# Kernel tuning notes

Hardware: AMD Instinct MI355X
Metric: run time of the kernel (lower is better)

## Reference

```python
import jax, jax.numpy as jnp
import numpy as np

TOPK_RATIO = 0.2
DICE_WEIGHT = 0.5
SHAPE = (2, 1, 128, 192, 192)


def setup_inputs() -> dict:
    key = jax.random.key(0)
    k1, k2 = jax.random.split(key)
    logits = jax.random.normal(k1, SHAPE, dtype=jnp.float32)
    targets = jax.random.uniform(k2, SHAPE, dtype=jnp.float32)
    return {"logits": logits, "targets": targets}


def _bce_with_logits(x, t):
    # stable: max(x,0) - x*t + log(1+exp(-|x|))
    return jnp.maximum(x, 0.0) - x * t + jnp.log1p(jnp.exp(-jnp.abs(x)))


def reference(logits, targets):
    # --- TopK BCE ---
    flat_loss = _bce_with_logits(logits, targets).reshape(-1)
    n = flat_loss.shape[0]
    k_samples = max(1, int(n * TOPK_RATIO))
    topk_losses, _ = jax.lax.top_k(flat_loss, k_samples)
    bce = jnp.mean(topk_losses)

    # --- Soft Dice ---
    p = jax.nn.sigmoid(logits).reshape(-1)
    t = targets.reshape(-1)
    intersection = jnp.sum(p * t)
    union = jnp.sum(p) + jnp.sum(t)
    dice = (2.0 * intersection + 1e-06) / (union + 1e-06)
    dice_loss = 1.0 - dice

    return bce + DICE_WEIGHT * dice_loss
```

## Files before the change

### kernel.cpp

```cpp
#include <hip/hip_runtime.h>
#include <math.h>
#include <limits.h>

#define NB1 8192
#define NB2 4096
#define VEC 4

__device__ __forceinline__ void elem_f(float x, float t, float& l, float& p) {
    float e = __expf(-fabsf(x));
    l = fmaxf(x, 0.f) - x * t + __logf(1.f + e);
    float r = __builtin_amdgcn_rcpf(1.f + e);
    p = (x >= 0.f) ? r : e * r;
}

__global__ __launch_bounds__(256) void sample_kernel(
    const float4* __restrict__ x4, const float4* __restrict__ t4,
    unsigned* __restrict__ H1, int n4)
{
    __shared__ unsigned lh[NB1];
    for (int i = threadIdx.x; i < NB1; i += 256) lh[i] = 0u;
    __syncthreads();
    int tid = blockIdx.x * 256 + threadIdx.x;
    int stride = gridDim.x * 256;
    int S4 = n4 >> 4;
    for (int i = tid; i < S4; i += stride) {
        int f4 = ((i >> 6) << 10) + (i & 63);
        if (f4 >= n4) continue;
        float4 xv = x4[f4];
        float4 tv = t4[f4];
        float xs[4] = {xv.x, xv.y, xv.z, xv.w};
        float ts[4] = {tv.x, tv.y, tv.z, tv.w};
        #pragma unroll
        for (int c = 0; c < 4; ++c) {
            float l, p;
            elem_f(xs[c], ts[c], l, p);
            atomicAdd(&lh[__float_as_uint(l) >> 19], 1u);
        }
    }
    __syncthreads();
    for (int i = threadIdx.x; i < NB1; i += 256) {
        unsigned c = lh[i];
        if (c) atomicAdd(&H1[i], c);
    }
}

__global__ __launch_bounds__(256) void band_kernel(
    const unsigned* __restrict__ H1, float* __restrict__ band,
    long long ks, long long M)
{
    __shared__ unsigned lh[NB1];
    const uint4* hv = (const uint4*)H1;
    uint4* lv = (uint4*)lh;
    for (int i = threadIdx.x; i < NB1 / 4; i += 256) lv[i] = hv[i];
    __syncthreads();
    if (threadIdx.x >= 64) return;

    int lane = threadIdx.x;
    int base = lane << 7;
    unsigned long long chunk = 0;
    for (int j = 0; j < 128; ++j) chunk += lh[base + j];
    unsigned long long s = chunk;
    #pragma unroll
    for (int off = 1; off < 64; off <<= 1) {
        unsigned long long v = __shfl_down(s, off);
        if (lane + off < 64) s += v;
    }
    unsigned long long above = s - chunk;

    int my_bhi = INT_MAX, my_blo = -1;
    unsigned long long c = above;
    for (int j = 127; j >= 0; --j) {
        unsigned h = lh[base + j];
        if ((long long)(c + h) < ks - M) my_bhi = base + j;
        if ((long long)c > ks + M && my_blo < 0) my_blo = base + j;
        c += h;
    }
    #pragma unroll
    for (int off = 32; off; off >>= 1) {
        int a = __shfl_down(my_bhi, off); my_bhi = min(my_bhi, a);
        int b = __shfl_down(my_blo, off); my_blo = max(my_blo, b);
    }
    if (lane == 0) {
        int bhi = (my_bhi == INT_MAX) ? (NB1 - 1) : my_bhi;
        int blo = my_blo;
        float vhi = __uint_as_float((unsigned)bhi << 19);
        float vlo = (blo < 0) ? 0.f : __uint_as_float((unsigned)(blo + 1) << 19);
        if (!(vlo < vhi)) vlo = 0.f;
        band[0] = vlo;
        band[1] = vhi;
    }
}

__device__ __forceinline__ void process4(
    float4 xv, float4 tv, float vlo, float vhi, float scale,
    float& sp, float& spt, float& st, float& sgt, unsigned& cnt,
    unsigned* __restrict__ hist2)
{
    float xs[4] = {xv.x, xv.y, xv.z, xv.w};
    float ts[4] = {tv.x, tv.y, tv.z, tv.w};
    #pragma unroll
    for (int c = 0; c < 4; ++c) {
        float l, p;
        elem_f(xs[c], ts[c], l, p);
        sp += p; spt += p * ts[c]; st += ts[c];
        if (l >= vhi) { cnt++; sgt += l; }
        else if (l >= vlo) {
            int b = min((int)((l - vlo) * scale), NB2 - 1);
            atomicAdd(&hist2[b], 1u);
        }
    }
}

__global__ __launch_bounds__(256, 8) void main_kernel(
    const float4* __restrict__ x4, const float4* __restrict__ t4,
    const float* __restrict__ band, unsigned* __restrict__ hist2,
    float* __restrict__ q0, float* __restrict__ q1,
    float* __restrict__ q2, float* __restrict__ q3, unsigned* __restrict__ qc,
    const float* __restrict__ xg, const float* __restrict__ tg,
    int n, int n4)
{
    float vlo = band[0], vhi = band[1];
    float scale = (float)NB2 / (vhi - vlo);

    int base = blockIdx.x * (256 * VEC) + threadIdx.x;
    float sp = 0.f, spt = 0.f, st = 0.f, sgt = 0.f;
    unsigned cnt = 0;

    bool full = (blockIdx.x + 1) * (256 * VEC) <= n4;
    if (full) {
        float4 xv[VEC], tv[VEC];
        #pragma unroll
        for (int j = 0; j < VEC; ++j) xv[j] = x4[base + j * 256];
        #pragma unroll
        for (int j = 0; j < VEC; ++j) tv[j] = t4[base + j * 256];
        #pragma unroll
        for (int j = 0; j < VEC; ++j)
            process4(xv[j], tv[j], vlo, vhi, scale, sp, spt, st, sgt, cnt, hist2);
    } else {
        for (int j = 0; j < VEC; ++j) {
            int idx = base + j * 256;
            if (idx < n4)
                process4(x4[idx], t4[idx], vlo, vhi, scale, sp, spt, st, sgt, cnt, hist2);
        }
    }
    int tail0 = n4 << 2;
    if (blockIdx.x == 0 && threadIdx.x < (n - tail0)) {
        float x = xg[tail0 + threadIdx.x], t = tg[tail0 + threadIdx.x];
        float l, p;
        elem_f(x, t, l, p);
        sp += p; spt += p * t; st += t;
        if (l >= vhi) { cnt++; sgt += l; }
        else if (l >= vlo) {
            int b = min((int)((l - vlo) * scale), NB2 - 1);
            atomicAdd(&hist2[b], 1u);
        }
    }

    #pragma unroll
    for (int off = 32; off; off >>= 1) {
        sp  += __shfl_down(sp,  off);
        spt += __shfl_down(spt, off);
        st  += __shfl_down(st,  off);
        sgt += __shfl_down(sgt, off);
        cnt += __shfl_down(cnt, off);
    }
    __shared__ float    rs[4][4];
    __shared__ unsigned rc[4];
    int w = threadIdx.x >> 6;
    if ((threadIdx.x & 63) == 0) {
        rs[w][0] = sp; rs[w][1] = spt; rs[w][2] = st; rs[w][3] = sgt; rc[w] = cnt;
    }
    __syncthreads();
    if (threadIdx.x == 0) {
        float a0 = 0, a1 = 0, a2 = 0, a3 = 0;
        unsigned c = 0;
        #pragma unroll
        for (int i = 0; i < 4; ++i) {
            a0 += rs[i][0]; a1 += rs[i][1]; a2 += rs[i][2]; a3 += rs[i][3]; c += rc[i];
        }
        q0[blockIdx.x] = a0; q1[blockIdx.x] = a1; q2[blockIdx.x] = a2;
        q3[blockIdx.x] = a3; qc[blockIdx.x] = c;
    }
}

__global__ __launch_bounds__(1024) void final_kernel(
    const unsigned* __restrict__ hist2, const float* __restrict__ band,
    const float* __restrict__ q0, const float* __restrict__ q1,
    const float* __restrict__ q2, const float* __restrict__ q3,
    const unsigned* __restrict__ qc, int nblocks,
    float* __restrict__ out, long long k)
{
    __shared__ unsigned lh[NB2];
    __shared__ double red[16][5];
    __shared__ double fin[5];

    for (int i = threadIdx.x; i < NB2; i += 1024) lh[i] = hist2[i];

    double a0 = 0, a1 = 0, a2 = 0, a3 = 0, a4 = 0;
    for (int i = threadIdx.x; i < nblocks; i += 1024) {
        a0 += (double)q0[i]; a1 += (double)q1[i]; a2 += (double)q2[i];
        a3 += (double)q3[i]; a4 += (double)qc[i];
    }
    #pragma unroll
    for (int off = 32; off; off >>= 1) {
        a0 += __shfl_down(a0, off); a1 += __shfl_down(a1, off);
        a2 += __shfl_down(a2, off); a3 += __shfl_down(a3, off);
        a4 += __shfl_down(a4, off);
    }
    int w = threadIdx.x >> 6;
    if ((threadIdx.x & 63) == 0) {
        red[w][0] = a0; red[w][1] = a1; red[w][2] = a2; red[w][3] = a3; red[w][4] = a4;
    }
    __syncthreads();
    if (threadIdx.x == 0) {
        double f0 = 0, f1 = 0, f2 = 0, f3 = 0, f4 = 0;
        for (int i = 0; i < 16; ++i) {
            f0 += red[i][0]; f1 += red[i][1]; f2 += red[i][2];
            f3 += red[i][3]; f4 += red[i][4];
        }
        fin[0] = f0; fin[1] = f1; fin[2] = f2; fin[3] = f3; fin[4] = f4;
    }
    __syncthreads();
    if (threadIdx.x >= 64) return;

    int lane = threadIdx.x;
    double SP = fin[0], SPT = fin[1], ST = fin[2], SGT = fin[3];
    long long CNT = (long long)fin[4];

    double vlo = (double)band[0], vhi = (double)band[1];
    double binw = (vhi - vlo) / NB2;
    long long k2 = k - CNT;

    int base = lane << 6;
    unsigned long long cchunk = 0;
    double wchunk = 0.0;
    for (int j = 0; j < 64; ++j) {
        unsigned h = lh[base + j];
        cchunk += h;
        wchunk += (double)h * (vlo + (base + j + 0.5) * binw);
    }
    unsigned long long cs = cchunk;
    double wsum = wchunk;
    #pragma unroll
    for (int off = 1; off < 64; off <<= 1) {
        unsigned long long cv = __shfl_down(cs, off);
        double wv = __shfl_down(wsum, off);
        if (lane + off < 64) { cs += cv; wsum += wv; }
    }
    unsigned long long total = __shfl(cs, 0);
    double wtotal = __shfl(wsum, 0);

    double I = SPT, U = SP + ST;
    double dice_part = 0.5 * (1.0 - (2.0 * I + 1e-6) / (U + 1e-6));

    if (k2 <= 0) {
        if (lane == 0) out[0] = (float)(SGT / (double)k + dice_part);
        return;
    }
    if ((unsigned long long)k2 > total) {
        if (lane == 0) {
            double sum_top = SGT + wtotal + (double)(k2 - (long long)total) * vlo;
            out[0] = (float)(sum_top / (double)k + dice_part);
        }
        return;
    }
    unsigned long long c = cs - cchunk;
    double wacc = wsum - wchunk;
    for (int j = 63; j >= 0; --j) {
        unsigned h = lh[base + j];
        double val = vlo + (base + j + 0.5) * binw;
        if (c < (unsigned long long)k2 && (unsigned long long)k2 <= c + h) {
            double sum_top = SGT + wacc + (double)((long long)k2 - (long long)c) * val;
            out[0] = (float)(sum_top / (double)k + dice_part);
        }
        c += h;
        wacc += (double)h * val;
    }
}

extern "C" void kernel_launch(void* const* d_in, const int* in_sizes, int n_in,
                              void* d_out, int out_size, void* d_ws, size_t ws_size,
                              hipStream_t stream)
{
    const float* x = (const float*)d_in[0];
    const float* t = (const float*)d_in[1];
    float* out = (float*)d_out;
    int n = in_sizes[0];
    int n4 = n >> 2;
    long long k = (long long)((double)n * 0.2);
    if (k < 1) k = 1;

    long long S = (long long)(n4 >> 4) * 4;
    long long ks = (S > 0) ? (long long)((double)k * (double)S / (double)n) : 0;
    long long M = 4096;

    int tilesz = 256 * VEC;
    int grid = (n4 + tilesz - 1) / tilesz;
    if (grid < 1) grid = 1;

    unsigned char* ws = (unsigned char*)d_ws;
    unsigned* H1    = (unsigned*)(ws);
    unsigned* hist2 = (unsigned*)(ws + 32768);
    float*    band  = (float*)(ws + 49152);
    size_t po = 50176;
    size_t pstride = (((size_t)grid * 4) + 255) & ~(size_t)255;
    float*    q0 = (float*)(ws + po);
    float*    q1 = (float*)(ws + po + pstride);
    float*    q2 = (float*)(ws + po + 2 * pstride);
    float*    q3 = (float*)(ws + po + 3 * pstride);
    unsigned* qc = (unsigned*)(ws + po + 4 * pstride);

    hipMemsetAsync(d_ws, 0, 49152, stream);

    sample_kernel<<<256, 256, 0, stream>>>((const float4*)x, (const float4*)t, H1, n4);
    band_kernel<<<1, 256, 0, stream>>>(H1, band, ks, M);
    main_kernel<<<grid, 256, 0, stream>>>((const float4*)x, (const float4*)t,
                                          band, hist2, q0, q1, q2, q3, qc, x, t, n, n4);
    final_kernel<<<1, 1024, 0, stream>>>(hist2, band, q0, q1, q2, q3, qc, grid, out, k);
}
```

Measured before the change: 138.5 us.

## Fuse band and final reductions into preceding kernels via last-block tickets

Merges the single-block band selection into the sampling kernel and the final reduction into the main kernel. Each uses an atomic ticket counter so only the last finishing block performs the serial tail work, reading the global results with agent-scope atomic loads. This removes two kernel launches and the gaps between them. In exchange every block pays a fence and an atomic, and the tail now runs as a 256-thread block inside a kernel tuned for occupancy rather than a dedicated 1024-thread launch.

```diff
diff --git a/kernel.cpp b/kernel.cpp
--- a/kernel.cpp
+++ b/kernel.cpp
@@ -13,9 +13,17 @@
     p = (x >= 0.f) ? r : e * r;
 }
 
-__global__ __launch_bounds__(256) void sample_kernel(
+__device__ __forceinline__ unsigned agent_load_u32(const unsigned* p) {
+    return __hip_atomic_load(p, __ATOMIC_RELAXED, __HIP_MEMORY_SCOPE_AGENT);
+}
+__device__ __forceinline__ float agent_load_f32(const float* p) {
+    return __hip_atomic_load(p, __ATOMIC_RELAXED, __HIP_MEMORY_SCOPE_AGENT);
+}
+
+__global__ __launch_bounds__(256) void sample_band_kernel(
     const float4* __restrict__ x4, const float4* __restrict__ t4,
-    unsigned* __restrict__ H1, int n4)
+    unsigned* __restrict__ H1, float* __restrict__ band,
+    unsigned* __restrict__ done, int n4, long long ks, long long M)
 {
     __shared__ unsigned lh[NB1];
     for (int i = threadIdx.x; i < NB1; i += 256) lh[i] = 0u;
@@ -42,16 +50,17 @@
         unsigned c = lh[i];
         if (c) atomicAdd(&H1[i], c);
     }
-}
-
-__global__ __launch_bounds__(256) void band_kernel(
-    const unsigned* __restrict__ H1, float* __restrict__ band,
-    long long ks, long long M)
-{
-    __shared__ unsigned lh[NB1];
-    const uint4* hv = (const uint4*)H1;
-    uint4* lv = (uint4*)lh;
-    for (int i = threadIdx.x; i < NB1 / 4; i += 256) lv[i] = hv[i];
+
+    __threadfence();
+    __syncthreads();
+    __shared__ unsigned ticket;
+    if (threadIdx.x == 0)
+        ticket = __hip_atomic_fetch_add(done, 1u, __ATOMIC_ACQ_REL, __HIP_MEMORY_SCOPE_AGENT);
+    __syncthreads();
+    if (ticket != gridDim.x - 1) return;
+    __threadfence();
+
+    for (int i = threadIdx.x; i < NB1; i += 256) lh[i] = agent_load_u32(&H1[i]);
     __syncthreads();
     if (threadIdx.x >= 64) return;
 
@@ -111,13 +120,14 @@
     }
 }
 
-__global__ __launch_bounds__(256, 8) void main_kernel(
+__global__ __launch_bounds__(256, 8) void main_final_kernel(
     const float4* __restrict__ x4, const float4* __restrict__ t4,
     const float* __restrict__ band, unsigned* __restrict__ hist2,
     float* __restrict__ q0, float* __restrict__ q1,
     float* __restrict__ q2, float* __restrict__ q3, unsigned* __restrict__ qc,
+    unsigned* __restrict__ done,
     const float* __restrict__ xg, const float* __restrict__ tg,
-    int n, int n4)
+    int n, int n4, float* __restrict__ out, long long k)
 {
     float vlo = band[0], vhi = band[1];
     float scale = (float)NB2 / (vhi - vlo);
@@ -181,25 +191,29 @@
         q0[blockIdx.x] = a0; q1[blockIdx.x] = a1; q2[blockIdx.x] = a2;
         q3[blockIdx.x] = a3; qc[blockIdx.x] = c;
     }
-}
-
-__global__ __launch_bounds__(1024) void final_kernel(
-    const unsigned* __restrict__ hist2, const float* __restrict__ band,
-    const float* __restrict__ q0, const float* __restrict__ q1,
-    const float* __restrict__ q2, const float* __restrict__ q3,
-    const unsigned* __restrict__ qc, int nblocks,
-    float* __restrict__ out, long long k)
-{
-    __shared__ unsigned lh[NB2];
-    __shared__ double red[16][5];
+
+    __threadfence();
+    __syncthreads();
+    __shared__ unsigned ticket;
+    if (threadIdx.x == 0)
+        ticket = __hip_atomic_fetch_add(done, 1u, __ATOMIC_ACQ_REL, __HIP_MEMORY_SCOPE_AGENT);
+    __syncthreads();
+    if (ticket != gridDim.x - 1) return;
+    __threadfence();
+
+    __shared__ unsigned lh2[NB2];
+    __shared__ double red[4][5];
     __shared__ double fin[5];
-
-    for (int i = threadIdx.x; i < NB2; i += 1024) lh[i] = hist2[i];
-
+    for (int i = threadIdx.x; i < NB2; i += 256) lh2[i] = agent_load_u32(&hist2[i]);
+
+    int nblocks = gridDim.x;
     double a0 = 0, a1 = 0, a2 = 0, a3 = 0, a4 = 0;
-    for (int i = threadIdx.x; i < nblocks; i += 1024) {
-        a0 += (double)q0[i]; a1 += (double)q1[i]; a2 += (double)q2[i];
-        a3 += (double)q3[i]; a4 += (double)qc[i];
+    for (int i = threadIdx.x; i < nblocks; i += 256) {
+        a0 += (double)agent_load_f32(&q0[i]);
+        a1 += (double)agent_load_f32(&q1[i]);
+        a2 += (double)agent_load_f32(&q2[i]);
+        a3 += (double)agent_load_f32(&q3[i]);
+        a4 += (double)agent_load_u32(&qc[i]);
     }
     #pragma unroll
     for (int off = 32; off; off >>= 1) {
@@ -207,14 +221,14 @@
         a2 += __shfl_down(a2, off); a3 += __shfl_down(a3, off);
         a4 += __shfl_down(a4, off);
     }
-    int w = threadIdx.x >> 6;
     if ((threadIdx.x & 63) == 0) {
         red[w][0] = a0; red[w][1] = a1; red[w][2] = a2; red[w][3] = a3; red[w][4] = a4;
     }
     __syncthreads();
     if (threadIdx.x == 0) {
         double f0 = 0, f1 = 0, f2 = 0, f3 = 0, f4 = 0;
-        for (int i = 0; i < 16; ++i) {
+        #pragma unroll
+        for (int i = 0; i < 4; ++i) {
             f0 += red[i][0]; f1 += red[i][1]; f2 += red[i][2];
             f3 += red[i][3]; f4 += red[i][4];
         }
@@ -227,17 +241,17 @@
     double SP = fin[0], SPT = fin[1], ST = fin[2], SGT = fin[3];
     long long CNT = (long long)fin[4];
 
-    double vlo = (double)band[0], vhi = (double)band[1];
-    double binw = (vhi - vlo) / NB2;
+    double dvlo = (double)vlo, dvhi = (double)vhi;
+    double binw = (dvhi - dvlo) / NB2;
     long long k2 = k - CNT;
 
-    int base = lane << 6;
+    int base2 = lane << 6;
     unsigned long long cchunk = 0;
     double wchunk = 0.0;
     for (int j = 0; j < 64; ++j) {
-        unsigned h = lh[base + j];
+        unsigned h = lh2[base2 + j];
         cchunk += h;
-        wchunk += (double)h * (vlo + (base + j + 0.5) * binw);
+        wchunk += (double)h * (dvlo + (base2 + j + 0.5) * binw);
     }
     unsigned long long cs = cchunk;
     double wsum = wchunk;
@@ -259,7 +273,7 @@
     }
     if ((unsigned long long)k2 > total) {
         if (lane == 0) {
-            double sum_top = SGT + wtotal + (double)(k2 - (long long)total) * vlo;
+            double sum_top = SGT + wtotal + (double)(k2 - (long long)total) * dvlo;
             out[0] = (float)(sum_top / (double)k + dice_part);
         }
         return;
@@ -267,8 +281,8 @@
     unsigned long long c = cs - cchunk;
     double wacc = wsum - wchunk;
     for (int j = 63; j >= 0; --j) {
-        unsigned h = lh[base + j];
-        double val = vlo + (base + j + 0.5) * binw;
+        unsigned h = lh2[base2 + j];
+        double val = dvlo + (base2 + j + 0.5) * binw;
         if (c < (unsigned long long)k2 && (unsigned long long)k2 <= c + h) {
             double sum_top = SGT + wacc + (double)((long long)k2 - (long long)c) * val;
             out[0] = (float)(sum_top / (double)k + dice_part);
@@ -302,7 +316,9 @@
     unsigned* H1    = (unsigned*)(ws);
     unsigned* hist2 = (unsigned*)(ws + 32768);
     float*    band  = (float*)(ws + 49152);
-    size_t po = 50176;
+    unsigned* done0 = (unsigned*)(ws + 49160);
+    unsigned* done1 = (unsigned*)(ws + 49164);
+    size_t po = 49408;
     size_t pstride = (((size_t)grid * 4) + 255) & ~(size_t)255;
     float*    q0 = (float*)(ws + po);
     float*    q1 = (float*)(ws + po + pstride);
@@ -310,11 +326,11 @@
     float*    q3 = (float*)(ws + po + 3 * pstride);
     unsigned* qc = (unsigned*)(ws + po + 4 * pstride);
 
-    hipMemsetAsync(d_ws, 0, 49152, stream);
-
-    sample_kernel<<<256, 256, 0, stream>>>((const float4*)x, (const float4*)t, H1, n4);
-    band_kernel<<<1, 256, 0, stream>>>(H1, band, ks, M);
-    main_kernel<<<grid, 256, 0, stream>>>((const float4*)x, (const float4*)t,
-                                          band, hist2, q0, q1, q2, q3, qc, x, t, n, n4);
-    final_kernel<<<1, 1024, 0, stream>>>(hist2, band, q0, q1, q2, q3, qc, grid, out, k);
-}
+    hipMemsetAsync(d_ws, 0, 49408, stream);
+
+    sample_band_kernel<<<256, 256, 0, stream>>>((const float4*)x, (const float4*)t,
+                                                H1, band, done0, n4, ks, M);
+    main_final_kernel<<<grid, 256, 0, stream>>>((const float4*)x, (const float4*)t,
+                                                band, hist2, q0, q1, q2, q3, qc, done1,
+                                                x, t, n, n4, out, k);
+}
```

After: 428.8 us. +209.7%, slower.

## Fuse sampling and band selection via last-block ticket; widen main-kernel tiles

Applied to the files above, without the earlier changes.

Merges the histogram sampling kernel and the single-block band kernel into one launch. The last block to finish, found with an atomic ticket counter, computes the band from the global histogram. The sample grid now launches one element per thread instead of a grid-stride loop, and overlaps the loads with the shared-memory clear. It also doubles VEC in the main kernel and lowers the occupancy hint from 8 to 4. This removes one kernel launch and serial gap at the cost of fence overhead and a tail that runs on a single block.

```diff
diff --git a/kernel.cpp b/kernel.cpp
--- a/kernel.cpp
+++ b/kernel.cpp
@@ -4,7 +4,7 @@
 
 #define NB1 8192
 #define NB2 4096
-#define VEC 4
+#define VEC 8
 
 __device__ __forceinline__ void elem_f(float x, float t, float& l, float& p) {
     float e = __expf(-fabsf(x));
@@ -13,27 +13,33 @@
     p = (x >= 0.f) ? r : e * r;
 }
 
-__global__ __launch_bounds__(256) void sample_kernel(
+__device__ __forceinline__ unsigned agent_load_u32(const unsigned* p) {
+    return __hip_atomic_load(p, __ATOMIC_RELAXED, __HIP_MEMORY_SCOPE_AGENT);
+}
+
+__global__ __launch_bounds__(256) void sample_band_kernel(
     const float4* __restrict__ x4, const float4* __restrict__ t4,
-    unsigned* __restrict__ H1, int n4)
+    unsigned* __restrict__ H1, float* __restrict__ band,
+    unsigned* __restrict__ done, int n4, long long ks, long long M)
 {
     __shared__ unsigned lh[NB1];
     for (int i = threadIdx.x; i < NB1; i += 256) lh[i] = 0u;
-    __syncthreads();
+
     int tid = blockIdx.x * 256 + threadIdx.x;
-    int stride = gridDim.x * 256;
     int S4 = n4 >> 4;
-    for (int i = tid; i < S4; i += stride) {
-        int f4 = ((i >> 6) << 10) + (i & 63);
-        if (f4 >= n4) continue;
-        float4 xv = x4[f4];
-        float4 tv = t4[f4];
-        float xs[4] = {xv.x, xv.y, xv.z, xv.w};
-        float ts[4] = {tv.x, tv.y, tv.z, tv.w};
+    bool v = tid < S4;
+    float4 xa, ta;
+    if (v) {
+        int f4 = ((tid >> 6) << 10) + (tid & 63);
+        xa = x4[f4]; ta = t4[f4];
+    }
+    __syncthreads();
+    if (v) {
+        float xs[4] = {xa.x, xa.y, xa.z, xa.w};
+        float ts[4] = {ta.x, ta.y, ta.z, ta.w};
         #pragma unroll
         for (int c = 0; c < 4; ++c) {
-            float l, p;
-            elem_f(xs[c], ts[c], l, p);
+            float l, p; elem_f(xs[c], ts[c], l, p);
             atomicAdd(&lh[__float_as_uint(l) >> 19], 1u);
         }
     }
@@ -42,16 +48,17 @@
         unsigned c = lh[i];
         if (c) atomicAdd(&H1[i], c);
     }
-}
-
-__global__ __launch_bounds__(256) void band_kernel(
-    const unsigned* __restrict__ H1, float* __restrict__ band,
-    long long ks, long long M)
-{
-    __shared__ unsigned lh[NB1];
-    const uint4* hv = (const uint4*)H1;
-    uint4* lv = (uint4*)lh;
-    for (int i = threadIdx.x; i < NB1 / 4; i += 256) lv[i] = hv[i];
+
+    __threadfence();
+    __syncthreads();
+    __shared__ unsigned ticket;
+    if (threadIdx.x == 0)
+        ticket = __hip_atomic_fetch_add(done, 1u, __ATOMIC_ACQ_REL, __HIP_MEMORY_SCOPE_AGENT);
+    __syncthreads();
+    if (ticket != gridDim.x - 1) return;
+    __threadfence();
+
+    for (int i = threadIdx.x; i < NB1; i += 256) lh[i] = agent_load_u32(&H1[i]);
     __syncthreads();
     if (threadIdx.x >= 64) return;
 
@@ -62,8 +69,8 @@
     unsigned long long s = chunk;
     #pragma unroll
     for (int off = 1; off < 64; off <<= 1) {
-        unsigned long long v = __shfl_down(s, off);
-        if (lane + off < 64) s += v;
+        unsigned long long vv = __shfl_down(s, off);
+        if (lane + off < 64) s += vv;
     }
     unsigned long long above = s - chunk;
 
@@ -111,7 +118,7 @@
     }
 }
 
-__global__ __launch_bounds__(256, 8) void main_kernel(
+__global__ __launch_bounds__(256, 4) void main_kernel(
     const float4* __restrict__ x4, const float4* __restrict__ t4,
     const float* __restrict__ band, unsigned* __restrict__ hist2,
     float* __restrict__ q0, float* __restrict__ q1,
@@ -298,10 +305,15 @@
     int grid = (n4 + tilesz - 1) / tilesz;
     if (grid < 1) grid = 1;
 
+    int S4 = n4 >> 4;
+    int sgrid = (S4 + 255) / 256;
+    if (sgrid < 1) sgrid = 1;
+
     unsigned char* ws = (unsigned char*)d_ws;
     unsigned* H1    = (unsigned*)(ws);
     unsigned* hist2 = (unsigned*)(ws + 32768);
     float*    band  = (float*)(ws + 49152);
+    unsigned* done0 = (unsigned*)(ws + 49160);
     size_t po = 50176;
     size_t pstride = (((size_t)grid * 4) + 255) & ~(size_t)255;
     float*    q0 = (float*)(ws + po);
@@ -310,10 +322,10 @@
     float*    q3 = (float*)(ws + po + 3 * pstride);
     unsigned* qc = (unsigned*)(ws + po + 4 * pstride);
 
-    hipMemsetAsync(d_ws, 0, 49152, stream);
-
-    sample_kernel<<<256, 256, 0, stream>>>((const float4*)x, (const float4*)t, H1, n4);
-    band_kernel<<<1, 256, 0, stream>>>(H1, band, ks, M);
+    hipMemsetAsync(d_ws, 0, 49408, stream);
+
+    sample_band_kernel<<<sgrid, 256, 0, stream>>>((const float4*)x, (const float4*)t,
+                                                  H1, band, done0, n4, ks, M);
     main_kernel<<<grid, 256, 0, stream>>>((const float4*)x, (const float4*)t,
                                           band, hist2, q0, q1, q2, q3, qc, x, t, n, n4);
     final_kernel<<<1, 1024, 0, stream>>>(hist2, band, q0, q1, q2, q3, qc, grid, out, k);
```

After: 186.2 us. 1.34x slower.
